# Optimization experiments

Measured on AMD Instinct MI355X. Metric: run time of the kernel, lower is better.

## Reference

```python
import jax, jax.numpy as jnp
import numpy as np

B, S, D = 8, 2048, 768

def setup_inputs() -> dict:
    key = jax.random.key(0)
    k1, k2, k3, k4 = jax.random.split(key, 4)
    x = jax.random.normal(k1, (B, S, D), dtype=jnp.float32)
    # torch Linear stores weight as [out, in] and computes x @ W^T; we store
    # pre-transposed [in, out] matrices so forward is x @ W.
    scale = 1.0 / np.sqrt(D)
    wq = jax.random.normal(k2, (D, D), dtype=jnp.float32) * scale
    wk = jax.random.normal(k3, (D, D), dtype=jnp.float32) * scale
    wv = jax.random.normal(k4, (D, D), dtype=jnp.float32) * scale
    return {"x": x, "wq": wq, "wk": wk, "wv": wv}

def reference(x, wq, wk, wv):
    d_out = wq.shape[1]
    q = jnp.einsum('bsd,de->bse', x, wq)
    k = jnp.einsum('bsd,de->bse', x, wk)
    v = jnp.einsum('bsd,de->bse', x, wv)
    # causal scores: note source scales by sqrt(d_out), not per-head dim
    scores = jnp.einsum('bqe,bke->bqk', q, k) / jnp.sqrt(jnp.float32(d_out))
    S_len = x.shape[1]
    causal = jnp.tril(jnp.ones((S_len, S_len), dtype=bool))  # True = keep
    scores = jnp.where(causal[None, :, :], scores, -jnp.inf)
    attn = jax.nn.softmax(scores, axis=-1)
    # dropout rate = 0.0 -> identity
    out = jnp.einsum('bqk,bke->bqe', attn, v)
    return out
```

## Files before the change

### kernel.cpp

```cpp
#include <hip/hip_runtime.h>
#include <hip/hip_bf16.h>

#define DI 768
#define SS 2048
#define QK_ELEMS ((size_t)16384 * 768)

typedef float f32x4 __attribute__((ext_vector_type(4)));
typedef short s16x8 __attribute__((ext_vector_type(8)));
typedef short s16x4 __attribute__((ext_vector_type(4)));

static __device__ __forceinline__ unsigned short f2bf(float f) {
    union { float f; unsigned int u; } a; a.f = f;
    unsigned int r = (a.u + 0x7FFFu + ((a.u >> 16) & 1u)) >> 16;
    return (unsigned short)r;
}

#define GLOAD_LDS16(SRC, DST) \
    __builtin_amdgcn_global_load_lds((const __attribute__((address_space(1))) unsigned int*)(SRC), \
                                     (__attribute__((address_space(3))) unsigned int*)(DST), 16, 0, 0)

__global__ __launch_bounds__(256) void conv_kernel(
    const float* __restrict__ x, unsigned short* __restrict__ xb)
{
    const size_t i = ((size_t)blockIdx.x * 256 + threadIdx.x) * 8;
    float4 a = *(const float4*)(x + i);
    float4 c = *(const float4*)(x + i + 4);
    ushort4 u0, u1;
    u0.x = f2bf(a.x); u0.y = f2bf(a.y); u0.z = f2bf(a.z); u0.w = f2bf(a.w);
    u1.x = f2bf(c.x); u1.y = f2bf(c.y); u1.z = f2bf(c.z); u1.w = f2bf(c.w);
    *(ushort4*)(xb + i) = u0;
    *(ushort4*)(xb + i + 4) = u1;
}

__global__ __launch_bounds__(256) void convw_kernel(
    const float* __restrict__ wq, const float* __restrict__ wk,
    const float* __restrict__ wv, unsigned short* __restrict__ wtb)
{
    __shared__ float tile[64][65];
    const int which = blockIdx.z;
    const float* w = (which == 0) ? wq : (which == 1) ? wk : wv;
    unsigned short* o = wtb + (size_t)which * DI * DI;
    const int k0 = blockIdx.x * 64, n0 = blockIdx.y * 64;
    const int tid = threadIdx.x;
    #pragma unroll
    for (int i = 0; i < 16; ++i) {
        int idx = tid + i * 256;
        int rr = idx >> 6, cc = idx & 63;
        tile[rr][cc] = w[(size_t)(k0 + rr) * DI + n0 + cc];
    }
    __syncthreads();
    #pragma unroll
    for (int i = 0; i < 16; ++i) {
        int idx = tid + i * 256;
        int rr = idx >> 6, cc = idx & 63;
        o[(size_t)(n0 + rr) * DI + k0 + cc] = f2bf(tile[cc][rr]);
    }
}

__global__ __launch_bounds__(256) void proj_kernel(
    const unsigned short* __restrict__ xb, const unsigned short* __restrict__ wtb,
    unsigned short* __restrict__ ws)
{
    __shared__ unsigned short As[128 * 32];
    __shared__ unsigned short Bs[128 * 32];

    const int which = blockIdx.z;
    const unsigned short* wt = wtb + (size_t)which * DI * DI;
    const int n0 = blockIdx.x * 128;
    const int m0 = blockIdx.y * 128;
    const int tid = threadIdx.x;
    const int lane = tid & 63, wid = tid >> 6;
    const int wr = wid >> 1, wc = wid & 1;
    const int r = lane & 15, g = lane >> 4;

    const int arow_l = lane >> 2;
    const int asrc_l = (((lane & 3) * 16) ^ ((arow_l & 1) << 5)) >> 1;

    f32x4 acc[4][4];
    #pragma unroll
    for (int i = 0; i < 4; ++i)
        #pragma unroll
        for (int j = 0; j < 4; ++j) acc[i][j] = (f32x4){0.f, 0.f, 0.f, 0.f};

    for (int k0 = 0; k0 < DI; k0 += 32) {
        #pragma unroll
        for (int ii = 0; ii < 2; ++ii) {
            const int idx = wid * 2 + ii;
            GLOAD_LDS16(xb + (size_t)(m0 + idx * 16 + arow_l) * DI + k0 + asrc_l,
                        &As[idx * 512]);
            GLOAD_LDS16(wt + (size_t)(n0 + idx * 16 + arow_l) * DI + k0 + asrc_l,
                        &Bs[idx * 512]);
        }
        __syncthreads();
        s16x8 af[4], bfr[4];
        #pragma unroll
        for (int fr = 0; fr < 4; ++fr) {
            const int arow = wr * 64 + fr * 16 + r;
            af[fr] = *(const s16x8*)((const char*)As + arow * 64 + ((g * 16) ^ ((arow & 1) << 5)));
        }
        #pragma unroll
        for (int cf = 0; cf < 4; ++cf) {
            const int brow = wc * 64 + cf * 16 + r;
            bfr[cf] = *(const s16x8*)((const char*)Bs + brow * 64 + ((g * 16) ^ ((brow & 1) << 5)));
        }
        #pragma unroll
        for (int fr = 0; fr < 4; ++fr)
            #pragma unroll
            for (int cf = 0; cf < 4; ++cf)
                acc[fr][cf] = __builtin_amdgcn_mfma_f32_16x16x32_bf16(af[fr], bfr[cf], acc[fr][cf], 0, 0, 0);
        __syncthreads();
    }

    const float scale = (which == 0) ? 0.03608439182435161f : 1.0f;
    if (which < 2) {
        unsigned short* O = ws + (size_t)which * QK_ELEMS;
        #pragma unroll
        for (int fr = 0; fr < 4; ++fr)
            #pragma unroll
            for (int cf = 0; cf < 4; ++cf) {
                int row = m0 + wr * 64 + fr * 16 + g * 4;
                int col = n0 + wc * 64 + cf * 16 + r;
                #pragma unroll
                for (int jj = 0; jj < 4; ++jj) {
                    int rr = row + jj;
                    int cc = col ^ ((rr & 7) << 3);
                    O[(size_t)rr * DI + cc] = f2bf(acc[fr][cf][jj] * scale);
                }
            }
    } else {
        unsigned short* O = ws + 2 * QK_ELEMS;
        #pragma unroll
        for (int fr = 0; fr < 4; ++fr)
            #pragma unroll
            for (int cf = 0; cf < 4; ++cf) {
                int row = m0 + wr * 64 + fr * 16 + g * 4;
                int bb = row >> 11;
                int st = (row & 2047) >> 4;
                int et = ((n0 + wc * 64) >> 4) + cf;
                ushort4 pk;
                pk.x = f2bf(acc[fr][cf][0]); pk.y = f2bf(acc[fr][cf][1]);
                pk.z = f2bf(acc[fr][cf][2]); pk.w = f2bf(acc[fr][cf][3]);
                *(ushort4*)&O[(((size_t)bb * 128 + st) * 48 + et) * 256 + lane * 4] = pk;
            }
    }
}

__global__ __launch_bounds__(512, 1) void attn_kernel(
    const unsigned short* __restrict__ ws, float* __restrict__ out)
{
    __shared__ unsigned short Ks[64 * 768];
    __shared__ unsigned short Qs[32 * 768];
    __shared__ unsigned short P_lds[2048];
    __shared__ float redm[128];

    const int id = blockIdx.x;
    const int b = id & 7;
    const int a = id >> 3;
    const int tid = threadIdx.x;
    const int wid = tid >> 6, lane = tid & 63;
    const int qsel = wid >> 2;
    const int wv = wid & 3;
    const int r = lane & 15, g = lane >> 4;
    const int et0 = wid * 6;
    const int rw = wv * 16 + r;
    const int swz = (r & 7) << 4;

    const unsigned short* Qb = ws + (size_t)b * SS * DI;
    const unsigned short* Kb = ws + QK_ELEMS + (size_t)b * SS * DI;
    const unsigned short* Vf = ws + 2 * QK_ELEMS + (size_t)b * 128 * 48 * 256;
    float* Ob = out + (size_t)b * SS * DI;
    const char* KsB = (const char*)Ks;
    const char* QsB = (const char*)Qs;

#define STAGEK(KT) do { \
        const size_t sbase_ = (size_t)(KT) * 64 * DI; \
        _Pragma("unroll") \
        for (int i_ = 0; i_ < 12; ++i_) { \
            const int idx_ = wid * 12 + i_; \
            GLOAD_LDS16(Kb + sbase_ + idx_ * 512 + lane * 8, &Ks[idx_ * 512]); \
        } \
    } while (0)

#define RAWBAR() do { \
        asm volatile("s_waitcnt lgkmcnt(0)" ::: "memory"); \
        __builtin_amdgcn_sched_barrier(0); \
        __builtin_amdgcn_s_barrier(); \
        __builtin_amdgcn_sched_barrier(0); \
    } while (0)

    for (int pp = 0; pp < 2; ++pp) {
        const int jbase = pp ? (126 - 2 * a) : (2 * a);
        const int q0 = (jbase + qsel) * 16;
        const int nt0 = (jbase * 16 + 79) >> 6;
        const int ntmax = ((jbase + 1) * 16 + 79) >> 6;
        const int nt_own = qsel ? ntmax : nt0;

        {
            const size_t qsb = (size_t)jbase * 16 * DI;
            #pragma unroll
            for (int i_ = 0; i_ < 6; ++i_) {
                const int idx_ = wid * 6 + i_;
                GLOAD_LDS16(Qb + qsb + idx_ * 512 + lane * 8, &Qs[idx_ * 512]);
            }
        }
        STAGEK(0);

        f32x4 acc[2][6];
        #pragma unroll
        for (int qs = 0; qs < 2; ++qs)
            #pragma unroll
            for (int cf = 0; cf < 6; ++cf) acc[qs][cf] = (f32x4){0.f, 0.f, 0.f, 0.f};
        float m0 = -1e30f, m1 = -1e30f, lp = 0.f;

        for (int kt = 0; kt < ntmax; ++kt) {
            const int k0 = kt * 64;
            const bool act0 = kt < nt0;
            const bool act_own = kt < nt_own;
            __syncthreads();

            s16x4 va[4][6];
            const size_t vbase = ((size_t)(k0 >> 4) * 48 + et0) * 256 + lane * 4;
            #pragma unroll
            for (int ks = 0; ks < 4; ++ks)
                #pragma unroll
                for (int cf = 0; cf < 6; ++cf)
                    va[ks][cf] = *(const s16x4*)(Vf + vbase + (size_t)ks * 48 * 256 + cf * 256);

            f32x4 s = {0.f, 0.f, 0.f, 0.f};
            if (act_own) {
                f32x4 sa = {0,0,0,0}, sb = {0,0,0,0};
                __builtin_amdgcn_s_setprio(1);
                #pragma unroll
                for (int t = 0; t < 24; t += 2) {
                    const int c0 = (t * 64 + g * 16) ^ swz;
                    const int c1 = (t * 64 + 64 + g * 16) ^ swz;
                    s16x8 qa  = *(const s16x8*)(QsB + qsel * 24576 + r * 1536 + c0);
                    s16x8 qb2 = *(const s16x8*)(QsB + qsel * 24576 + r * 1536 + c1);
                    s16x8 ka  = *(const s16x8*)(KsB + rw * 1536 + c0);
                    s16x8 kb2 = *(const s16x8*)(KsB + rw * 1536 + c1);
                    sa = __builtin_amdgcn_mfma_f32_16x16x32_bf16(ka,  qa,  sa, 0, 0, 0);
                    sb = __builtin_amdgcn_mfma_f32_16x16x32_bf16(kb2, qb2, sb, 0, 0, 0);
                }
                __builtin_amdgcn_s_setprio(0);
                #pragma unroll
                for (int jj = 0; jj < 4; ++jj) s[jj] = sa[jj] + sb[jj];
                if (k0 + 64 > q0) {
                    #pragma unroll
                    for (int jj = 0; jj < 4; ++jj)
                        if (k0 + 16 * wv + 4 * g + jj > q0 + r) s[jj] = -1e30f;
                }
                float v = fmaxf(fmaxf(s[0], s[1]), fmaxf(s[2], s[3]));
                v = fmaxf(v, __shfl_xor(v, 16));
                v = fmaxf(v, __shfl_xor(v, 32));
                if (lane < 16) redm[qsel * 64 + wv * 16 + lane] = v;
            }
            RAWBAR();

            if (kt + 1 < ntmax) STAGEK(kt + 1);

            {
                float vm1 = fmaxf(fmaxf(redm[64 + r], redm[80 + r]),
                                  fmaxf(redm[96 + r], redm[112 + r]));
                float vm0 = act0 ? fmaxf(fmaxf(redm[r], redm[16 + r]),
                                         fmaxf(redm[32 + r], redm[48 + r])) : -1e30f;
                bool need = __any(vm1 > m1 + 8.0f) || (act0 && __any(vm0 > m0 + 8.0f));
                if (need) {
                    const float mn0 = fmaxf(m0, vm0), mn1 = fmaxf(m1, vm1);
                    const float a0 = __expf(m0 - mn0), a1 = __expf(m1 - mn1);
                    m0 = mn0; m1 = mn1;
                    lp *= qsel ? a1 : a0;
                    float al0[4], al1[4];
                    #pragma unroll
                    for (int jj = 0; jj < 4; ++jj) {
                        al0[jj] = __shfl(a0, 4 * g + jj);
                        al1[jj] = __shfl(a1, 4 * g + jj);
                    }
                    #pragma unroll
                    for (int cf = 0; cf < 6; ++cf)
                        #pragma unroll
                        for (int jj = 0; jj < 4; ++jj) {
                            acc[0][cf][jj] *= al0[jj];
                            acc[1][cf][jj] *= al1[jj];
                        }
                }
                if (act_own) {
                    const float mo = qsel ? m1 : m0;
                    s16x4 pw;
                    #pragma unroll
                    for (int jj = 0; jj < 4; ++jj) {
                        float p = __expf(s[jj] - mo);
                        lp += p;
                        pw[jj] = (short)f2bf(p);
                    }
                    *(s16x4*)&P_lds[qsel * 1024 + wv * 256 + r * 16 + g * 4] = pw;
                }
            }
            RAWBAR();

            {
                s16x4 pa0[4], pa1[4];
                #pragma unroll
                for (int ks = 0; ks < 4; ++ks) {
                    pa0[ks] = *(const s16x4*)&P_lds[ks * 256 + r * 16 + g * 4];
                    pa1[ks] = *(const s16x4*)&P_lds[1024 + ks * 256 + r * 16 + g * 4];
                }
                __builtin_amdgcn_s_setprio(1);
                if (act0) {
                    #pragma unroll
                    for (int cf = 0; cf < 6; ++cf)
                        #pragma unroll
                        for (int ks = 0; ks < 4; ++ks)
                            acc[0][cf] = __builtin_amdgcn_mfma_f32_16x16x16bf16_1k(pa0[ks], va[ks][cf], acc[0][cf], 0, 0, 0);
                }
                #pragma unroll
                for (int cf = 0; cf < 6; ++cf)
                    #pragma unroll
                    for (int ks = 0; ks < 4; ++ks)
                        acc[1][cf] = __builtin_amdgcn_mfma_f32_16x16x16bf16_1k(pa1[ks], va[ks][cf], acc[1][cf], 0, 0, 0);
                __builtin_amdgcn_s_setprio(0);
            }
        }
        lp += __shfl_xor(lp, 16);
        lp += __shfl_xor(lp, 32);
        if (lane < 16) redm[qsel * 64 + wv * 16 + lane] = lp;
        __syncthreads();
        const float lt0 = redm[r] + redm[16 + r] + redm[32 + r] + redm[48 + r];
        const float lt1 = redm[64 + r] + redm[80 + r] + redm[96 + r] + redm[112 + r];
        const float li0 = 1.0f / lt0, li1 = 1.0f / lt1;
        float lv0[4], lv1[4];
        #pragma unroll
        for (int jj = 0; jj < 4; ++jj) {
            lv0[jj] = __shfl(li0, 4 * g + jj);
            lv1[jj] = __shfl(li1, 4 * g + jj);
        }
        #pragma unroll
        for (int cf = 0; cf < 6; ++cf)
            #pragma unroll
            for (int jj = 0; jj < 4; ++jj) {
                Ob[(size_t)(jbase * 16 + 4 * g + jj) * DI + wid * 96 + cf * 16 + r] = acc[0][cf][jj] * lv0[jj];
                Ob[(size_t)((jbase + 1) * 16 + 4 * g + jj) * DI + wid * 96 + cf * 16 + r] = acc[1][cf][jj] * lv1[jj];
            }
        __syncthreads();
    }
#undef STAGEK
#undef RAWBAR
}

extern "C" void kernel_launch(void* const* d_in, const int* in_sizes, int n_in,
                              void* d_out, int out_size, void* d_ws, size_t ws_size,
                              hipStream_t stream) {
    const float* x  = (const float*)d_in[0];
    const float* wq = (const float*)d_in[1];
    const float* wk = (const float*)d_in[2];
    const float* wv = (const float*)d_in[3];
    unsigned short* ws = (unsigned short*)d_ws;
    float* out = (float*)d_out;
    unsigned short* xb  = (unsigned short*)d_out;
    unsigned short* wtb = (unsigned short*)d_out + QK_ELEMS;

    conv_kernel<<<(int)(QK_ELEMS / (256 * 8)), 256, 0, stream>>>(x, xb);
    convw_kernel<<<dim3(12, 12, 3), 256, 0, stream>>>(wq, wk, wv, wtb);
    proj_kernel<<<dim3(6, 128, 3), 256, 0, stream>>>(xb, wtb, ws);
    attn_kernel<<<256, 512, 0, stream>>>(ws, out);
}
```

Before: 261.4 us.

## Compute QK scores with 32x32x16 MFMA on two waves instead of eight

The QK^T score computation moves from 16x16x32 MFMAs spread across all eight waves (each doing a 16x16 tile) to 32x32x16 MFMAs on only two waves, each covering 32 queries by 32 keys. This cuts the LDS fragment reads per output element and the number of row-max reduction partials, and the P tile layout and denominator reduction are rewritten to match. In exchange, six waves sit idle during the score phase, which could lengthen the critical path. The per-wave inactive-tile skipping for the lower query block is also dropped, so masking alone now handles those tiles.

```diff
diff --git a/kernel.cpp b/kernel.cpp
--- a/kernel.cpp
+++ b/kernel.cpp
@@ -6,6 +6,7 @@
 #define QK_ELEMS ((size_t)16384 * 768)
 
 typedef float f32x4 __attribute__((ext_vector_type(4)));
+typedef float f32x16 __attribute__((ext_vector_type(16)));
 typedef short s16x8 __attribute__((ext_vector_type(8)));
 typedef short s16x4 __attribute__((ext_vector_type(4)));
 
@@ -158,12 +159,9 @@
     const int a = id >> 3;
     const int tid = threadIdx.x;
     const int wid = tid >> 6, lane = tid & 63;
-    const int qsel = wid >> 2;
-    const int wv = wid & 3;
+    const int qkw = (wid == 0) ? 0 : (wid == 2) ? 1 : -1;
     const int r = lane & 15, g = lane >> 4;
     const int et0 = wid * 6;
-    const int rw = wv * 16 + r;
-    const int swz = (r & 7) << 4;
 
     const unsigned short* Qb = ws + (size_t)b * SS * DI;
     const unsigned short* Kb = ws + QK_ELEMS + (size_t)b * SS * DI;
@@ -190,10 +188,8 @@
 
     for (int pp = 0; pp < 2; ++pp) {
         const int jbase = pp ? (126 - 2 * a) : (2 * a);
-        const int q0 = (jbase + qsel) * 16;
         const int nt0 = (jbase * 16 + 79) >> 6;
         const int ntmax = ((jbase + 1) * 16 + 79) >> 6;
-        const int nt_own = qsel ? ntmax : nt0;
 
         {
             const size_t qsb = (size_t)jbase * 16 * DI;
@@ -212,10 +208,17 @@
             for (int cf = 0; cf < 6; ++cf) acc[qs][cf] = (f32x4){0.f, 0.f, 0.f, 0.f};
         float m0 = -1e30f, m1 = -1e30f, lp = 0.f;
 
+        const int ql = lane & 31;
+        const int h  = lane >> 5;
+        const int krow = (qkw > 0 ? 32 : 0) + ql;
+        const char* kbp = KsB + krow * 1536;
+        const int kswz = (krow & 7) << 4;
+        const char* qbp = QsB + ql * 1536;
+        const int qswz2 = (ql & 7) << 4;
+
         for (int kt = 0; kt < ntmax; ++kt) {
             const int k0 = kt * 64;
             const bool act0 = kt < nt0;
-            const bool act_own = kt < nt_own;
             __syncthreads();
 
             s16x4 va[4][6];
@@ -226,49 +229,48 @@
                 for (int cf = 0; cf < 6; ++cf)
                     va[ks][cf] = *(const s16x4*)(Vf + vbase + (size_t)ks * 48 * 256 + cf * 256);
 
-            f32x4 s = {0.f, 0.f, 0.f, 0.f};
-            if (act_own) {
-                f32x4 sa = {0,0,0,0}, sb = {0,0,0,0};
+            float sv[16];
+            if (qkw >= 0) {
+                f32x16 sA, sB;
+                #pragma unroll
+                for (int i2 = 0; i2 < 16; ++i2) { sA[i2] = 0.f; sB[i2] = 0.f; }
                 __builtin_amdgcn_s_setprio(1);
                 #pragma unroll
-                for (int t = 0; t < 24; t += 2) {
-                    const int c0 = (t * 64 + g * 16) ^ swz;
-                    const int c1 = (t * 64 + 64 + g * 16) ^ swz;
-                    s16x8 qa  = *(const s16x8*)(QsB + qsel * 24576 + r * 1536 + c0);
-                    s16x8 qb2 = *(const s16x8*)(QsB + qsel * 24576 + r * 1536 + c1);
-                    s16x8 ka  = *(const s16x8*)(KsB + rw * 1536 + c0);
-                    s16x8 kb2 = *(const s16x8*)(KsB + rw * 1536 + c1);
-                    sa = __builtin_amdgcn_mfma_f32_16x16x32_bf16(ka,  qa,  sa, 0, 0, 0);
-                    sb = __builtin_amdgcn_mfma_f32_16x16x32_bf16(kb2, qb2, sb, 0, 0, 0);
+                for (int t = 0; t < 48; t += 2) {
+                    s16x8 kf0 = *(const s16x8*)(kbp + ((t * 32 + h * 16) ^ kswz));
+                    s16x8 qf0 = *(const s16x8*)(qbp + ((t * 32 + h * 16) ^ qswz2));
+                    s16x8 kf1 = *(const s16x8*)(kbp + (((t + 1) * 32 + h * 16) ^ kswz));
+                    s16x8 qf1 = *(const s16x8*)(qbp + (((t + 1) * 32 + h * 16) ^ qswz2));
+                    sA = __builtin_amdgcn_mfma_f32_32x32x16_bf16(kf0, qf0, sA, 0, 0, 0);
+                    sB = __builtin_amdgcn_mfma_f32_32x32x16_bf16(kf1, qf1, sB, 0, 0, 0);
                 }
                 __builtin_amdgcn_s_setprio(0);
-                #pragma unroll
-                for (int jj = 0; jj < 4; ++jj) s[jj] = sa[jj] + sb[jj];
-                if (k0 + 64 > q0) {
-                    #pragma unroll
-                    for (int jj = 0; jj < 4; ++jj)
-                        if (k0 + 16 * wv + 4 * g + jj > q0 + r) s[jj] = -1e30f;
-                }
-                float v = fmaxf(fmaxf(s[0], s[1]), fmaxf(s[2], s[3]));
-                v = fmaxf(v, __shfl_xor(v, 16));
-                v = fmaxf(v, __shfl_xor(v, 32));
-                if (lane < 16) redm[qsel * 64 + wv * 16 + lane] = v;
+                const int qg = jbase * 16 + ql;
+                float vmx = -1e30f;
+                #pragma unroll
+                for (int i2 = 0; i2 < 16; ++i2) {
+                    float s_ = sA[i2] + sB[i2];
+                    const int kg = k0 + (qkw > 0 ? 32 : 0) + (i2 & 3) + 8 * (i2 >> 2) + 4 * h;
+                    if (kg > qg) s_ = -1e30f;
+                    sv[i2] = s_;
+                    vmx = fmaxf(vmx, s_);
+                }
+                vmx = fmaxf(vmx, __shfl_xor(vmx, 32));
+                if (lane < 32) redm[qkw * 32 + lane] = vmx;
             }
             RAWBAR();
 
             if (kt + 1 < ntmax) STAGEK(kt + 1);
 
             {
-                float vm1 = fmaxf(fmaxf(redm[64 + r], redm[80 + r]),
-                                  fmaxf(redm[96 + r], redm[112 + r]));
-                float vm0 = act0 ? fmaxf(fmaxf(redm[r], redm[16 + r]),
-                                         fmaxf(redm[32 + r], redm[48 + r])) : -1e30f;
-                bool need = __any(vm1 > m1 + 8.0f) || (act0 && __any(vm0 > m0 + 8.0f));
+                float vm0 = fmaxf(redm[r], redm[32 + r]);
+                float vm1 = fmaxf(redm[16 + r], redm[48 + r]);
+                bool need = __any(vm0 > m0 + 8.0f) || __any(vm1 > m1 + 8.0f);
                 if (need) {
                     const float mn0 = fmaxf(m0, vm0), mn1 = fmaxf(m1, vm1);
                     const float a0 = __expf(m0 - mn0), a1 = __expf(m1 - mn1);
                     m0 = mn0; m1 = mn1;
-                    lp *= qsel ? a1 : a0;
+                    lp *= (ql < 16) ? a0 : a1;
                     float al0[4], al1[4];
                     #pragma unroll
                     for (int jj = 0; jj < 4; ++jj) {
@@ -283,16 +285,22 @@
                             acc[1][cf][jj] *= al1[jj];
                         }
                 }
-                if (act_own) {
-                    const float mo = qsel ? m1 : m0;
-                    s16x4 pw;
-                    #pragma unroll
-                    for (int jj = 0; jj < 4; ++jj) {
-                        float p = __expf(s[jj] - mo);
-                        lp += p;
-                        pw[jj] = (short)f2bf(p);
+                if (qkw >= 0) {
+                    const float mo = (ql < 16) ? m0 : m1;
+                    const int qsl = ql >> 4;
+                    #pragma unroll
+                    for (int G = 0; G < 4; ++G) {
+                        s16x4 pw;
+                        #pragma unroll
+                        for (int jj = 0; jj < 4; ++jj) {
+                            float p = __expf(sv[4 * G + jj] - mo);
+                            lp += p;
+                            pw[jj] = (short)f2bf(p);
+                        }
+                        const int slice = qkw * 2 + (G >> 1);
+                        const int koff = (G & 1) * 8 + 4 * h;
+                        *(s16x4*)&P_lds[qsl * 1024 + slice * 256 + (lane & 15) * 16 + koff] = pw;
                     }
-                    *(s16x4*)&P_lds[qsel * 1024 + wv * 256 + r * 16 + g * 4] = pw;
                 }
             }
             RAWBAR();
@@ -320,12 +328,13 @@
                 __builtin_amdgcn_s_setprio(0);
             }
         }
-        lp += __shfl_xor(lp, 16);
-        lp += __shfl_xor(lp, 32);
-        if (lane < 16) redm[qsel * 64 + wv * 16 + lane] = lp;
+        if (qkw >= 0) {
+            lp += __shfl_xor(lp, 32);
+            if (lane < 32) redm[qkw * 32 + lane] = lp;
+        }
         __syncthreads();
-        const float lt0 = redm[r] + redm[16 + r] + redm[32 + r] + redm[48 + r];
-        const float lt1 = redm[64 + r] + redm[80 + r] + redm[96 + r] + redm[112 + r];
+        const float lt0 = redm[r] + redm[32 + r];
+        const float lt1 = redm[16 + r] + redm[48 + r];
         const float li0 = 1.0f / lt0, li1 = 1.0f / lt1;
         float lv0[4], lv1[4];
         #pragma unroll
```

Result: slower. 274.4 us (+5.0%).
